# Optimization experiments

Measured on AMD Instinct MI355X. Metric: run time of the kernel, lower is better.

The kernel has to match this reference:

```python
import jax, jax.numpy as jnp
import numpy as np

N = 20000      # atoms
E = 320000     # edges
F = 128        # node_size (hard-pinned by split(128) / expand to 384)
RBF = 20
RC = 5.0
ITERS = 3
NM = 64        # molecules in batch


def setup_inputs() -> dict:
    key = jax.random.key(0)
    ks = iter(jax.random.split(key, 64))
    def nrm(shape, scale=0.05):
        return jax.random.normal(next(ks), shape, dtype=jnp.float32) * scale
    inp = {}
    inp["z"] = jax.random.randint(next(ks), (N,), 0, 119)
    inp["graph"] = jax.random.randint(next(ks), (E, 2), 0, N)
    inp["edges_dist"] = jax.random.uniform(next(ks), (E,), minval=0.5, maxval=RC, dtype=jnp.float32)
    sense = jax.random.normal(next(ks), (E, 3), dtype=jnp.float32)
    inp["edges_sense"] = sense / jnp.linalg.norm(sense, axis=1, keepdims=True)
    inp["graph_idx"] = jnp.sort(jax.random.randint(next(ks), (N,), 0, NM))
    # parameters (stacked over ITERS message/update blocks)
    inp["emb"] = nrm((119, F), 1.0)
    inp["mw1"] = nrm((ITERS, F, F)); inp["mb1"] = nrm((ITERS, F))
    inp["mw2"] = nrm((ITERS, 3 * F, F)); inp["mb2"] = nrm((ITERS, 3 * F))
    inp["ew"] = nrm((ITERS, 3 * F, RBF)); inp["eb"] = nrm((ITERS, 3 * F))
    inp["uw"] = nrm((ITERS, F, F)); inp["vw"] = nrm((ITERS, F, F))
    inp["aw1"] = nrm((ITERS, F, 2 * F)); inp["ab1"] = nrm((ITERS, F))
    inp["aw2"] = nrm((ITERS, 3 * F, F)); inp["ab2"] = nrm((ITERS, 3 * F))
    inp["ow1"] = nrm((F, F)); inp["ob1"] = nrm((F,))
    inp["ow2"] = nrm((1, F)); inp["ob2"] = nrm((1,))
    return inp


def reference(z, graph, edges_dist, edges_sense, graph_idx,
              emb, mw1, mb1, mw2, mb2, ew, eb,
              uw, vw, aw1, ab1, aw2, ab2, ow1, ob1, ow2, ob2):
    src = graph[:, 0]   # scatter target (index_add index)
    dst = graph[:, 1]   # gather source (neighbour)
    s = emb[z]                                  # [N, F]
    v = jnp.zeros((N, 3, F), dtype=s.dtype)     # [N, 3, F]
    # edge-level precompute (same every iteration)
    n = jnp.arange(1, RBF + 1, dtype=jnp.float32)
    d = edges_dist[:, None]
    rbf = jnp.sin(n * jnp.pi * d / RC) / d                              # [E, RBF]
    cut = 0.5 * (jnp.cos(jnp.pi * edges_dist / RC) + 1.0) * (edges_dist < RC)  # [E]
    for i in range(ITERS):
        # --- Message block ---
        a = jax.nn.silu(s @ mw1[i].T + mb1[i]) @ mw2[i].T + mb2[i]      # [N, 3F]
        dist_rep = (rbf @ ew[i].T + eb[i]) * cut[:, None]               # [E, 3F]
        res = a[dst] * dist_rep                                         # [E, 3F]
        rv, rs, rd = res[:, :F], res[:, F:2 * F], res[:, 2 * F:]
        resv = v[dst] * rv[:, None, :] + edges_sense[:, :, None] * rd[:, None, :]  # [E,3,F]
        s = s + 2.0 * jax.ops.segment_sum(rs, src, num_segments=N)
        v = v + 2.0 * jax.ops.segment_sum(resv, src, num_segments=N)
        # --- Update block ---
        Uv = v @ uw[i].T                                                # [N,3,F]
        Vv = v @ vw[i].T
        h = jnp.concatenate([s, jnp.linalg.norm(Vv, axis=1)], axis=-1)  # [N, 2F]
        a2 = jax.nn.silu(h @ aw1[i].T + ab1[i]) @ aw2[i].T + ab2[i]     # [N, 3F]
        avv, asv, ass = a2[:, :F], a2[:, F:2 * F], a2[:, 2 * F:]
        s = s + ass + asv * jnp.sum(Uv * Vv, axis=1)
        v = v + avv[:, None, :] * Uv
    out = jax.nn.silu(s @ ow1.T + ob1) @ ow2.T + ob2                    # [N, 1]
    return jax.ops.segment_sum(out, graph_idx, num_segments=NM)         # [NM, 1]
```

## Files before the change

### kernel.cpp

```cpp
#include <hip/hip_runtime.h>
#include <math.h>

#define NN 20000
#define NE 320000
#define FD 128
#define RBFN 20
#define RC_ 5.0f
#define NITER 3
#define NMOL 64
#define F3 384
#define F2 256
#define PI_ 3.14159265358979323846f
#define KB 128
#define LPAD 8
#define SDS 392

typedef __attribute__((ext_vector_type(8))) short  bf16x8;
typedef __attribute__((ext_vector_type(4))) float  floatx4;
typedef unsigned short u16;
typedef unsigned int   u32;

__device__ __forceinline__ u16 f2b(float x) {
    union { float f; unsigned int u; } v; v.f = x;
    unsigned int u = v.u;
    return (u16)((u + 0x7fffu + ((u >> 16) & 1u)) >> 16);
}
__device__ __forceinline__ float b2f(u16 x) {
    union { unsigned int u; float f; } v; v.u = ((unsigned int)x) << 16;
    return v.f;
}
__device__ __forceinline__ float blo(u32 w) {
    union { unsigned int u; float f; } v; v.u = w << 16; return v.f;
}
__device__ __forceinline__ float bhi(u32 w) {
    union { unsigned int u; float f; } v; v.u = w & 0xffff0000u; return v.f;
}
__device__ __forceinline__ u32 pack2(float a, float b) {
    return (u32)f2b(a) | ((u32)f2b(b) << 16);
}

__global__ __launch_bounds__(256) void cvt_w_kernel(
    const float* s0, int n0, const float* s1, int n1, const float* s2, int n2,
    const float* s3, int n3, const float* s4, int n4, const float* s5, int n5,
    const float* s6, int n6, u16* __restrict__ dst)
{
    int idx = blockIdx.x * 256 + threadIdx.x;
    if (idx < n0) { dst[idx] = f2b(s0[idx]); return; } idx -= n0; dst += n0;
    if (idx < n1) { dst[idx] = f2b(s1[idx]); return; } idx -= n1; dst += n1;
    if (idx < n2) { dst[idx] = f2b(s2[idx]); return; } idx -= n2; dst += n2;
    if (idx < n3) { dst[idx] = f2b(s3[idx]); return; } idx -= n3; dst += n3;
    if (idx < n4) { dst[idx] = f2b(s4[idx]); return; } idx -= n4; dst += n4;
    if (idx < n5) { dst[idx] = f2b(s5[idx]); return; } idx -= n5; dst += n5;
    if (idx < n6) { dst[idx] = f2b(s6[idx]); }
}

__global__ __launch_bounds__(256) void cvt_ew_kernel(const float* __restrict__ ew,
    u16* __restrict__ ewb)
{
    int idx = blockIdx.x * 256 + threadIdx.x;
    if (idx >= NITER * F3 * 32) return;
    int k = idx & 31;
    int row = idx >> 5;
    ewb[idx] = (k < RBFN) ? f2b(ew[row * RBFN + k]) : (u16)0;
}

__global__ __launch_bounds__(256) void init_kernel(const int* __restrict__ z,
    const float* __restrict__ emb, float* __restrict__ s, u16* __restrict__ sbf,
    float* __restrict__ v_a, int* __restrict__ v_pk_i)
{
    int idx = blockIdx.x * 256 + threadIdx.x;
    if (idx < NN * F3) v_a[idx] = 0.f;
    if (idx < NN * F3 / 2) v_pk_i[idx] = 0;
    if (idx < NN * FD) {
        int n = idx >> 7, f = idx & 127;
        float v = emb[z[n] * FD + f];
        s[idx] = v; sbf[idx] = f2b(v);
    }
}

__global__ __launch_bounds__(256) void zero_i_kernel(int* __restrict__ p, int n)
{
    int idx = blockIdx.x * 256 + threadIdx.x;
    if (idx < n) p[idx] = 0;
}

__global__ __launch_bounds__(256) void csr_count_kernel(const int* __restrict__ graph,
    int* __restrict__ cnt)
{
    int e = blockIdx.x * 256 + threadIdx.x;
    if (e >= NE) return;
    atomicAdd(&cnt[graph[2 * e]], 1);
}

__global__ __launch_bounds__(1024) void csr_scan_kernel(const int* __restrict__ cnt,
    int* __restrict__ row_ptr, int* __restrict__ cursor)
{
    __shared__ int sd[1024];
    int tid = threadIdx.x;
    const int chunk = (NN + 1023) / 1024;
    int start = tid * chunk;
    int end = start + chunk; if (end > NN) end = NN;
    int sum = 0;
    for (int j = start; j < end; j++) sum += cnt[j];
    sd[tid] = sum;
    __syncthreads();
    for (int off = 1; off < 1024; off <<= 1) {
        int v = 0;
        if (tid >= off) v = sd[tid - off];
        __syncthreads();
        if (tid >= off) sd[tid] += v;
        __syncthreads();
    }
    int run = (tid == 0) ? 0 : sd[tid - 1];
    for (int j = start; j < end; j++) {
        row_ptr[j] = run;
        cursor[j]  = run;
        run += cnt[j];
    }
    if (tid == 0) row_ptr[NN] = NE;
}

__global__ __launch_bounds__(256) void csr_scatter_kernel(const int* __restrict__ graph,
    int* __restrict__ cursor, int* __restrict__ edge_list)
{
    int e = blockIdx.x * 256 + threadIdx.x;
    if (e >= NE) return;
    int p = atomicAdd(&cursor[graph[2 * e]], 1);
    edge_list[p] = e;
}

__global__ __launch_bounds__(256) void edge_stream_kernel(
    const int* __restrict__ edge_list, const int* __restrict__ graph,
    const float* __restrict__ dist, const float* __restrict__ sense,
    u16* __restrict__ rbf_bf, float* __restrict__ cut_p,
    float* __restrict__ sense_p, int* __restrict__ dst_p)
{
    int j = blockIdx.x * 256 + threadIdx.x;
    if (j >= NE) return;
    int e = edge_list[j];
    float d = dist[e];
    float inv = 1.f / d;
    float base = PI_ * d / RC_;
    float s1, c1;
    __sincosf(base, &s1, &c1);
    float twoc = c1 + c1;
    u16* rb = rbf_bf + (size_t)j * 32;
    float sprev = 0.f, scur = s1;
    #pragma unroll
    for (int k = 0; k < RBFN; k++) {
        rb[k] = f2b(scur * inv);
        float snext = twoc * scur - sprev;
        sprev = scur; scur = snext;
    }
    #pragma unroll
    for (int k = RBFN; k < 32; k++) rb[k] = 0;
    cut_p[j] = 0.5f * (c1 + 1.f) * (d < RC_ ? 1.f : 0.f);
    dst_p[j] = graph[2 * e + 1];
    sense_p[3 * j + 0] = sense[3 * e + 0];
    sense_p[3 * j + 1] = sense[3 * e + 1];
    sense_p[3 * j + 2] = sense[3 * e + 2];
}

template<int K1, bool PACK>
__global__ __launch_bounds__(256) void mlp_kernel(const u16* __restrict__ A,
    const u16* __restrict__ W1, const float* __restrict__ b1,
    const u16* __restrict__ W2, const float* __restrict__ b2,
    u16* __restrict__ Ob, int M)
{
    __shared__ u16 As[64][KB + LPAD];
    __shared__ u16 Ws[128][KB + LPAD];
    __shared__ u16 T[64][KB + LPAD];
    const int bm = blockIdx.x * 64;
    const int tid = threadIdx.x;
    const int wave = tid >> 6, lane = tid & 63;
    const int wm  = (wave >> 1) * 32;
    const int wn1 = (wave & 1) * 64;
    const int wn  = (wave & 1) * 32;
    const int quad = lane >> 4, lr = lane & 15;
    const int r = tid >> 2, q = tid & 3;

    floatx4 acc1[2][4];
    #pragma unroll
    for (int i = 0; i < 2; i++)
        #pragma unroll
        for (int j = 0; j < 4; j++) acc1[i][j] = (floatx4)0.f;

    for (int ko = 0; ko < K1; ko += KB) {
        {
            int gm = bm + r;
            u16* dA = &As[r][q * 32];
            if (gm < M) {
                const u16* ap = A + (size_t)gm * K1 + ko + q * 32;
                #pragma unroll
                for (int x = 0; x < 32; x += 8)
                    *(bf16x8*)&dA[x] = *(const bf16x8*)(ap + x);
            } else {
                #pragma unroll
                for (int x = 0; x < 32; x += 8)
                    *(bf16x8*)&dA[x] = (bf16x8)0;
            }
            #pragma unroll
            for (int h = 0; h < 2; h++) {
                int wr = r + h * 64;
                const u16* wp = W1 + (size_t)wr * K1 + ko + q * 32;
                u16* dW = &Ws[wr][q * 32];
                #pragma unroll
                for (int x = 0; x < 32; x += 8)
                    *(bf16x8*)&dW[x] = *(const bf16x8*)(wp + x);
            }
        }
        __syncthreads();
        #pragma unroll
        for (int kk = 0; kk < KB; kk += 32) {
            bf16x8 a0 = *(const bf16x8*)&As[wm + lr     ][kk + quad * 8];
            bf16x8 a1 = *(const bf16x8*)&As[wm + 16 + lr][kk + quad * 8];
            #pragma unroll
            for (int j = 0; j < 4; j++) {
                bf16x8 b = *(const bf16x8*)&Ws[wn1 + j * 16 + lr][kk + quad * 8];
                acc1[0][j] = __builtin_amdgcn_mfma_f32_16x16x32_bf16(a0, b, acc1[0][j], 0, 0, 0);
                acc1[1][j] = __builtin_amdgcn_mfma_f32_16x16x32_bf16(a1, b, acc1[1][j], 0, 0, 0);
            }
        }
        __syncthreads();
    }
    #pragma unroll
    for (int i = 0; i < 2; i++) {
        #pragma unroll
        for (int j = 0; j < 4; j++) {
            int col = wn1 + j * 16 + lr;
            float bb = b1[col];
            #pragma unroll
            for (int rr = 0; rr < 4; rr++) {
                int row = wm + i * 16 + quad * 4 + rr;
                float v = acc1[i][j][rr] + bb;
                v = v / (1.f + __expf(-v));
                T[row][col] = f2b(v);
            }
        }
    }
    __syncthreads();

    for (int c0 = 0; c0 < F3; c0 += 64) {
        {
            const u16* wp = W2 + (size_t)(c0 + r) * KB + q * 32;
            u16* dW = &Ws[r][q * 32];
            #pragma unroll
            for (int x = 0; x < 32; x += 8)
                *(bf16x8*)&dW[x] = *(const bf16x8*)(wp + x);
        }
        __syncthreads();
        floatx4 acc2[2][2];
        #pragma unroll
        for (int i = 0; i < 2; i++)
            #pragma unroll
            for (int j = 0; j < 2; j++) acc2[i][j] = (floatx4)0.f;
        #pragma unroll
        for (int kk = 0; kk < KB; kk += 32) {
            bf16x8 a0 = *(const bf16x8*)&T[wm + lr     ][kk + quad * 8];
            bf16x8 a1 = *(const bf16x8*)&T[wm + 16 + lr][kk + quad * 8];
            bf16x8 b0 = *(const bf16x8*)&Ws[wn + lr     ][kk + quad * 8];
            bf16x8 b1 = *(const bf16x8*)&Ws[wn + 16 + lr][kk + quad * 8];
            acc2[0][0] = __builtin_amdgcn_mfma_f32_16x16x32_bf16(a0, b0, acc2[0][0], 0, 0, 0);
            acc2[0][1] = __builtin_amdgcn_mfma_f32_16x16x32_bf16(a0, b1, acc2[0][1], 0, 0, 0);
            acc2[1][0] = __builtin_amdgcn_mfma_f32_16x16x32_bf16(a1, b0, acc2[1][0], 0, 0, 0);
            acc2[1][1] = __builtin_amdgcn_mfma_f32_16x16x32_bf16(a1, b1, acc2[1][1], 0, 0, 0);
        }
        #pragma unroll
        for (int i = 0; i < 2; i++) {
            #pragma unroll
            for (int j = 0; j < 2; j++) {
                int gn = c0 + wn + j * 16 + lr;
                float bb = b2[gn];
                #pragma unroll
                for (int rr = 0; rr < 4; rr++) {
                    int gm = bm + wm + i * 16 + quad * 4 + rr;
                    if (gm < M) {
                        u16 val = f2b(acc2[i][j][rr] + bb);
                        if (PACK) {
                            int off = (gn < 256) ? ((gn & 127) * 2 + (gn >> 7))
                                                 : (256 + (gn & 127));
                            Ob[(size_t)gm * F3 + off] = val;
                        } else {
                            Ob[(size_t)gm * F3 + gn] = val;
                        }
                    }
                }
            }
        }
        __syncthreads();
    }
}

__global__ __launch_bounds__(256) void gemm_uv(const u16* __restrict__ A,
    const u16* __restrict__ Wu, const u16* __restrict__ Wv,
    u16* __restrict__ U, u16* __restrict__ V, int M)
{
    __shared__ u16 As[64][KB + LPAD];
    __shared__ u16 Bu[64][KB + LPAD];
    __shared__ u16 Bv[64][KB + LPAD];
    const int bm = blockIdx.x * 64;
    const int bn = blockIdx.y * 64;
    const int tid = threadIdx.x;
    const int r = tid >> 2;
    const int q = tid & 3;
    const int wave = tid >> 6;
    const int lane = tid & 63;
    const int wm = (wave >> 1) * 32;
    const int wn = (wave & 1) * 32;
    const int quad = lane >> 4;
    const int lr = lane & 15;

    floatx4 au[2][2], av[2][2];
    #pragma unroll
    for (int i = 0; i < 2; i++)
        #pragma unroll
        for (int j = 0; j < 2; j++) { au[i][j] = (floatx4)0.f; av[i][j] = (floatx4)0.f; }

    {
        int gm = bm + r;
        u16* dA = &As[r][q * 32];
        if (gm < M) {
            const u16* ap = A + (size_t)gm * KB + q * 32;
            #pragma unroll
            for (int x = 0; x < 32; x += 8)
                *(bf16x8*)&dA[x] = *(const bf16x8*)(ap + x);
        } else {
            #pragma unroll
            for (int x = 0; x < 32; x += 8)
                *(bf16x8*)&dA[x] = (bf16x8)0;
        }
        int gn = bn + r;
        const u16* up = Wu + (size_t)gn * KB + q * 32;
        const u16* vp = Wv + (size_t)gn * KB + q * 32;
        u16* dU = &Bu[r][q * 32];
        u16* dV = &Bv[r][q * 32];
        #pragma unroll
        for (int x = 0; x < 32; x += 8) {
            *(bf16x8*)&dU[x] = *(const bf16x8*)(up + x);
            *(bf16x8*)&dV[x] = *(const bf16x8*)(vp + x);
        }
    }
    __syncthreads();
    #pragma unroll
    for (int kk = 0; kk < KB; kk += 32) {
        bf16x8 a0 = *(const bf16x8*)&As[wm + lr     ][kk + quad * 8];
        bf16x8 a1 = *(const bf16x8*)&As[wm + 16 + lr][kk + quad * 8];
        bf16x8 u0 = *(const bf16x8*)&Bu[wn + lr     ][kk + quad * 8];
        bf16x8 u1 = *(const bf16x8*)&Bu[wn + 16 + lr][kk + quad * 8];
        bf16x8 v0 = *(const bf16x8*)&Bv[wn + lr     ][kk + quad * 8];
        bf16x8 v1 = *(const bf16x8*)&Bv[wn + 16 + lr][kk + quad * 8];
        au[0][0] = __builtin_amdgcn_mfma_f32_16x16x32_bf16(a0, u0, au[0][0], 0, 0, 0);
        au[0][1] = __builtin_amdgcn_mfma_f32_16x16x32_bf16(a0, u1, au[0][1], 0, 0, 0);
        au[1][0] = __builtin_amdgcn_mfma_f32_16x16x32_bf16(a1, u0, au[1][0], 0, 0, 0);
        au[1][1] = __builtin_amdgcn_mfma_f32_16x16x32_bf16(a1, u1, au[1][1], 0, 0, 0);
        av[0][0] = __builtin_amdgcn_mfma_f32_16x16x32_bf16(a0, v0, av[0][0], 0, 0, 0);
        av[0][1] = __builtin_amdgcn_mfma_f32_16x16x32_bf16(a0, v1, av[0][1], 0, 0, 0);
        av[1][0] = __builtin_amdgcn_mfma_f32_16x16x32_bf16(a1, v0, av[1][0], 0, 0, 0);
        av[1][1] = __builtin_amdgcn_mfma_f32_16x16x32_bf16(a1, v1, av[1][1], 0, 0, 0);
    }
    #pragma unroll
    for (int i = 0; i < 2; i++) {
        #pragma unroll
        for (int j = 0; j < 2; j++) {
            int gn = bn + wn + j * 16 + lr;
            #pragma unroll
            for (int rr = 0; rr < 4; rr++) {
                int gm = bm + wm + i * 16 + quad * 4 + rr;
                if (gm < M) {
                    U[(size_t)gm * FD + gn] = f2b(au[i][j][rr]);
                    V[(size_t)gm * FD + gn] = f2b(av[i][j][rr]);
                }
            }
        }
    }
}

__global__ __launch_bounds__(256) void edge_mfma_kernel(
    const u16* __restrict__ rbf_bf, const float* __restrict__ cut_p,
    const float* __restrict__ sense_p, const int* __restrict__ dst_p,
    const u16* __restrict__ ewb, const float* __restrict__ eb,
    const u16* __restrict__ a_pk, const float* __restrict__ s_in,
    const float* __restrict__ v_in, const u16* __restrict__ v_pk,
    const int* __restrict__ row_ptr,
    float* __restrict__ s_out, u16* __restrict__ s_obf,
    float* __restrict__ v_out, u16* __restrict__ v_obf)
{
    __shared__ u16   sdrep[16 * SDS];
    __shared__ float scut[16];
    __shared__ float ssen[16][4];
    __shared__ int   sdst[16];
    __shared__ float red[4 * 128];

    const int n = blockIdx.x;
    const int tid = threadIdx.x;
    const int wave = tid >> 6;
    const int lane = tid & 63;
    const int quad = lane >> 4;
    const int lr = lane & 15;
    const int f = tid & 127;
    const int half = tid >> 7;

    int beg = row_ptr[n], end = row_ptr[n + 1];
    float accs = 0.f, accv0 = 0.f, accv1 = 0.f, accv2 = 0.f;

    for (int t0 = beg; t0 < end; t0 += 16) {
        int cnt = end - t0; if (cnt > 16) cnt = 16;
        __syncthreads();
        if (tid < 16) {
            scut[tid] = (tid < cnt) ? cut_p[t0 + tid] : 0.f;
            sdst[tid] = (tid < cnt) ? dst_p[t0 + tid] : 0;
        }
        if (tid >= 64 && tid < 64 + 3 * cnt) {
            int x = tid - 64;
            ssen[x / 3][x % 3] = sense_p[3 * t0 + x];
        }
        bf16x8 afrag;
        int ge = t0 + lr;
        if (ge < end) afrag = *(const bf16x8*)&rbf_bf[(size_t)ge * 32 + quad * 8];
        else          afrag = (bf16x8)0;
        floatx4 dacc[6];
        #pragma unroll
        for (int nt = 0; nt < 6; nt++) {
            int nrow = (wave * 6 + nt) * 16 + lr;
            bf16x8 bfrag = *(const bf16x8*)&ewb[(size_t)nrow * 32 + quad * 8];
            dacc[nt] = __builtin_amdgcn_mfma_f32_16x16x32_bf16(afrag, bfrag, (floatx4)0.f, 0, 0, 0);
        }
        __syncthreads();
        #pragma unroll
        for (int nt = 0; nt < 6; nt++) {
            int ncol = (wave * 6 + nt) * 16 + lr;
            float ebn = eb[ncol];
            #pragma unroll
            for (int rr = 0; rr < 4; rr++) {
                int e = quad * 4 + rr;
                sdrep[e * SDS + ncol] = f2b((dacc[nt][rr] + ebn) * scut[e]);
            }
        }
        __syncthreads();
        int nh = cnt - half * 8; if (nh > 8) nh = 8;
        for (int k = 0; k < nh; k++) {
            int e = half * 8 + k;
            int dst = sdst[e];
            const u16* sr = &sdrep[e * SDS];
            float drv = b2f(sr[f]);
            float drs = b2f(sr[FD + f]);
            float drd = b2f(sr[2 * FD + f]);
            const u16* ar = a_pk + (size_t)dst * F3;
            u32 ap = *(const u32*)(ar + f * 2);
            float rv = b2f((u16)(ap & 0xffff)) * drv;
            float rs = b2f((u16)(ap >> 16))    * drs;
            float rd = b2f(ar[256 + f])        * drd;
            accs += rs;
            const u16* vr = v_pk + (size_t)dst * F3;
            u32 vp = *(const u32*)(vr + f * 2);
            accv0 += b2f((u16)(vp & 0xffff)) * rv + ssen[e][0] * rd;
            accv1 += b2f((u16)(vp >> 16))    * rv + ssen[e][1] * rd;
            accv2 += b2f(vr[256 + f])        * rv + ssen[e][2] * rd;
        }
    }
    __syncthreads();
    if (half == 1) {
        red[f] = accs; red[128 + f] = accv0; red[256 + f] = accv1; red[384 + f] = accv2;
    }
    __syncthreads();
    if (half == 0) {
        accs  += red[f];       accv0 += red[128 + f];
        accv1 += red[256 + f]; accv2 += red[384 + f];
        int nb = n * FD + f;
        float so = s_in[nb] + 2.f * accs;
        s_out[nb] = so; s_obf[nb] = f2b(so);
        int vb = n * F3 + f;
        float w0 = v_in[vb]           + 2.f * accv0;
        float w1 = v_in[vb + FD]      + 2.f * accv1;
        float w2 = v_in[vb + 2 * FD]  + 2.f * accv2;
        v_out[vb]          = w0; v_obf[vb]          = f2b(w0);
        v_out[vb + FD]     = w1; v_obf[vb + FD]     = f2b(w1);
        v_out[vb + 2 * FD] = w2; v_obf[vb + 2 * FD] = f2b(w2);
    }
}

__global__ __launch_bounds__(256) void mlp2_update_kernel(
    const u16* __restrict__ sbf_mid, const float* __restrict__ s_mid,
    const float* __restrict__ v_mid,
    const u16* __restrict__ Uv, const u16* __restrict__ Vv,
    const u16* __restrict__ W1, const float* __restrict__ b1,
    const u16* __restrict__ W2, const float* __restrict__ b2,
    float* __restrict__ s_out, u16* __restrict__ s_obf,
    float* __restrict__ v_out, u16* __restrict__ v_pk, int M)
{
    __shared__ u16 As[64][KB + LPAD];
    __shared__ u16 Ws[128][KB + LPAD];
    __shared__ u16 T[64][KB + LPAD];
    const int bm = blockIdx.x * 64;
    const int tid = threadIdx.x;
    const int wave = tid >> 6, lane = tid & 63;
    const int wm  = (wave >> 1) * 32;
    const int wn1 = (wave & 1) * 64;
    const int wn  = (wave & 1) * 32;
    const int quad = lane >> 4, lr = lane & 15;
    const int r = tid >> 2, q = tid & 3;

    floatx4 acc1[2][4];
    #pragma unroll
    for (int i = 0; i < 2; i++)
        #pragma unroll
        for (int j = 0; j < 4; j++) acc1[i][j] = (floatx4)0.f;

    {
        int gm = bm + r;
        u16* dA = &As[r][q * 32];
        if (gm < M) {
            const u16* ap = sbf_mid + (size_t)gm * FD + q * 32;
            #pragma unroll
            for (int x = 0; x < 32; x += 8)
                *(bf16x8*)&dA[x] = *(const bf16x8*)(ap + x);
        } else {
            #pragma unroll
            for (int x = 0; x < 32; x += 8)
                *(bf16x8*)&dA[x] = (bf16x8)0;
        }
        #pragma unroll
        for (int h = 0; h < 2; h++) {
            int wr = r + h * 64;
            const u16* wp = W1 + (size_t)wr * F2 + q * 32;
            u16* dW = &Ws[wr][q * 32];
            #pragma unroll
            for (int x = 0; x < 32; x += 8)
                *(bf16x8*)&dW[x] = *(const bf16x8*)(wp + x);
        }
    }
    __syncthreads();
    #pragma unroll
    for (int kk = 0; kk < KB; kk += 32) {
        bf16x8 a0 = *(const bf16x8*)&As[wm + lr     ][kk + quad * 8];
        bf16x8 a1 = *(const bf16x8*)&As[wm + 16 + lr][kk + quad * 8];
        #pragma unroll
        for (int j = 0; j < 4; j++) {
            bf16x8 b = *(const bf16x8*)&Ws[wn1 + j * 16 + lr][kk + quad * 8];
            acc1[0][j] = __builtin_amdgcn_mfma_f32_16x16x32_bf16(a0, b, acc1[0][j], 0, 0, 0);
            acc1[1][j] = __builtin_amdgcn_mfma_f32_16x16x32_bf16(a1, b, acc1[1][j], 0, 0, 0);
        }
    }
    __syncthreads();
    {
        int gm = bm + r;
        u16* dA = &As[r][q * 32];
        if (gm < M) {
            const u16* vvp = Vv + (size_t)gm * F3 + q * 32;
            bf16x8 c0[4], c1[4], c2[4];
            #pragma unroll
            for (int t = 0; t < 4; t++) {
                c0[t] = *(const bf16x8*)(vvp + t * 8);
                c1[t] = *(const bf16x8*)(vvp + FD + t * 8);
                c2[t] = *(const bf16x8*)(vvp + 2 * FD + t * 8);
            }
            #pragma unroll
            for (int t = 0; t < 4; t++) {
                #pragma unroll
                for (int x = 0; x < 8; x++) {
                    float a = b2f((u16)c0[t][x]);
                    float b = b2f((u16)c1[t][x]);
                    float c = b2f((u16)c2[t][x]);
                    dA[t * 8 + x] = f2b(sqrtf(a * a + b * b + c * c));
                }
            }
        } else {
            #pragma unroll
            for (int x = 0; x < 32; x += 8)
                *(bf16x8*)&dA[x] = (bf16x8)0;
        }
        #pragma unroll
        for (int h = 0; h < 2; h++) {
            int wr = r + h * 64;
            const u16* wp = W1 + (size_t)wr * F2 + KB + q * 32;
            u16* dW = &Ws[wr][q * 32];
            #pragma unroll
            for (int x = 0; x < 32; x += 8)
                *(bf16x8*)&dW[x] = *(const bf16x8*)(wp + x);
        }
    }
    __syncthreads();
    #pragma unroll
    for (int kk = 0; kk < KB; kk += 32) {
        bf16x8 a0 = *(const bf16x8*)&As[wm + lr     ][kk + quad * 8];
        bf16x8 a1 = *(const bf16x8*)&As[wm + 16 + lr][kk + quad * 8];
        #pragma unroll
        for (int j = 0; j < 4; j++) {
            bf16x8 b = *(const bf16x8*)&Ws[wn1 + j * 16 + lr][kk + quad * 8];
            acc1[0][j] = __builtin_amdgcn_mfma_f32_16x16x32_bf16(a0, b, acc1[0][j], 0, 0, 0);
            acc1[1][j] = __builtin_amdgcn_mfma_f32_16x16x32_bf16(a1, b, acc1[1][j], 0, 0, 0);
        }
    }
    __syncthreads();
    #pragma unroll
    for (int i = 0; i < 2; i++) {
        #pragma unroll
        for (int j = 0; j < 4; j++) {
            int col = wn1 + j * 16 + lr;
            float bb = b1[col];
            #pragma unroll
            for (int rr = 0; rr < 4; rr++) {
                int row = wm + i * 16 + quad * 4 + rr;
                float v = acc1[i][j][rr] + bb;
                v = v / (1.f + __expf(-v));
                T[row][col] = f2b(v);
            }
        }
    }
    __syncthreads();

    float avvr[2][2][4], asvr[2][2][4];
    #pragma unroll
    for (int part = 0; part < 2; part++) {
        #pragma unroll
        for (int piece = 0; piece < 3; piece++) {
            const int c0 = piece * 128 + part * 64;
            {
                const u16* wp = W2 + (size_t)(c0 + r) * KB + q * 32;
                u16* dW = &Ws[r][q * 32];
                #pragma unroll
                for (int x = 0; x < 32; x += 8)
                    *(bf16x8*)&dW[x] = *(const bf16x8*)(wp + x);
            }
            __syncthreads();
            floatx4 acc2[2][2];
            #pragma unroll
            for (int i = 0; i < 2; i++)
                #pragma unroll
                for (int j = 0; j < 2; j++) acc2[i][j] = (floatx4)0.f;
            #pragma unroll
            for (int kk = 0; kk < KB; kk += 32) {
                bf16x8 a0 = *(const bf16x8*)&T[wm + lr     ][kk + quad * 8];
                bf16x8 a1 = *(const bf16x8*)&T[wm + 16 + lr][kk + quad * 8];
                bf16x8 b0 = *(const bf16x8*)&Ws[wn + lr     ][kk + quad * 8];
                bf16x8 b1 = *(const bf16x8*)&Ws[wn + 16 + lr][kk + quad * 8];
                acc2[0][0] = __builtin_amdgcn_mfma_f32_16x16x32_bf16(a0, b0, acc2[0][0], 0, 0, 0);
                acc2[0][1] = __builtin_amdgcn_mfma_f32_16x16x32_bf16(a0, b1, acc2[0][1], 0, 0, 0);
                acc2[1][0] = __builtin_amdgcn_mfma_f32_16x16x32_bf16(a1, b0, acc2[1][0], 0, 0, 0);
                acc2[1][1] = __builtin_amdgcn_mfma_f32_16x16x32_bf16(a1, b1, acc2[1][1], 0, 0, 0);
            }
            if (piece == 0) {
                #pragma unroll
                for (int i = 0; i < 2; i++)
                    #pragma unroll
                    for (int j = 0; j < 2; j++) {
                        int gn = c0 + wn + j * 16 + lr;
                        float bb = b2[gn];
                        #pragma unroll
                        for (int rr = 0; rr < 4; rr++)
                            avvr[i][j][rr] = acc2[i][j][rr] + bb;
                    }
            } else if (piece == 1) {
                #pragma unroll
                for (int i = 0; i < 2; i++)
                    #pragma unroll
                    for (int j = 0; j < 2; j++) {
                        int gn = c0 + wn + j * 16 + lr;
                        float bb = b2[gn];
                        #pragma unroll
                        for (int rr = 0; rr < 4; rr++)
                            asvr[i][j][rr] = acc2[i][j][rr] + bb;
                    }
            } else {
                #pragma unroll
                for (int i = 0; i < 2; i++) {
                    #pragma unroll
                    for (int j = 0; j < 2; j++) {
                        int gn = c0 + wn + j * 16 + lr;
                        int f  = gn - 256;
                        float bb = b2[gn];
                        #pragma unroll
                        for (int rr = 0; rr < 4; rr++) {
                            int gm = bm + wm + i * 16 + quad * 4 + rr;
                            if (gm < M) {
                                float ass = acc2[i][j][rr] + bb;
                                float asv = asvr[i][j][rr];
                                float avv = avvr[i][j][rr];
                                int vb = gm * F3 + f;
                                float u0 = b2f(Uv[vb]);
                                float u1 = b2f(Uv[vb + FD]);
                                float u2 = b2f(Uv[vb + 2 * FD]);
                                float w0 = b2f(Vv[vb]);
                                float w1 = b2f(Vv[vb + FD]);
                                float w2 = b2f(Vv[vb + 2 * FD]);
                                float dot = u0 * w0 + u1 * w1 + u2 * w2;
                                int nb = gm * FD + f;
                                float so = s_mid[nb] + ass + asv * dot;
                                s_out[nb] = so; s_obf[nb] = f2b(so);
                                float y0 = v_mid[vb]          + avv * u0;
                                float y1 = v_mid[vb + FD]     + avv * u1;
                                float y2 = v_mid[vb + 2 * FD] + avv * u2;
                                v_out[vb]          = y0;
                                v_out[vb + FD]     = y1;
                                v_out[vb + 2 * FD] = y2;
                                char* vpb = (char*)v_pk + (size_t)gm * (2 * F3);
                                *(u32*)(vpb + 4 * f) = pack2(y0, y1);
                                *(u16*)(vpb + 512 + 2 * f) = f2b(y2);
                            }
                        }
                    }
                }
            }
            __syncthreads();
        }
    }
}

__global__ __launch_bounds__(256) void head_kernel(const u16* __restrict__ A,
    const u16* __restrict__ W1, const float* __restrict__ b1,
    const float* __restrict__ ow2, const float* __restrict__ ob2,
    float* __restrict__ nodeval)
{
    __shared__ u16 As[64][KB + LPAD];
    __shared__ u16 Ws[128][KB + LPAD];
    __shared__ float T[64][KB + 4];
    __shared__ float ow2s[KB];
    const int bm = blockIdx.x * 64;
    const int tid = threadIdx.x;
    const int wave = tid >> 6, lane = tid & 63;
    const int wm  = (wave >> 1) * 32;
    const int wn1 = (wave & 1) * 64;
    const int quad = lane >> 4, lr = lane & 15;
    const int r = tid >> 2, q = tid & 3;

    if (tid < KB) ow2s[tid] = ow2[tid];

    floatx4 acc1[2][4];
    #pragma unroll
    for (int i = 0; i < 2; i++)
        #pragma unroll
        for (int j = 0; j < 4; j++) acc1[i][j] = (floatx4)0.f;

    {
        int gm = bm + r;
        u16* dA = &As[r][q * 32];
        if (gm < NN) {
            const u16* ap = A + (size_t)gm * KB + q * 32;
            #pragma unroll
            for (int x = 0; x < 32; x += 8)
                *(bf16x8*)&dA[x] = *(const bf16x8*)(ap + x);
        } else {
            #pragma unroll
            for (int x = 0; x < 32; x += 8)
                *(bf16x8*)&dA[x] = (bf16x8)0;
        }
        #pragma unroll
        for (int h = 0; h < 2; h++) {
            int wr = r + h * 64;
            const u16* wp = W1 + (size_t)wr * KB + q * 32;
            u16* dW = &Ws[wr][q * 32];
            #pragma unroll
            for (int x = 0; x < 32; x += 8)
                *(bf16x8*)&dW[x] = *(const bf16x8*)(wp + x);
        }
    }
    __syncthreads();
    #pragma unroll
    for (int kk = 0; kk < KB; kk += 32) {
        bf16x8 a0 = *(const bf16x8*)&As[wm + lr     ][kk + quad * 8];
        bf16x8 a1 = *(const bf16x8*)&As[wm + 16 + lr][kk + quad * 8];
        #pragma unroll
        for (int j = 0; j < 4; j++) {
            bf16x8 b = *(const bf16x8*)&Ws[wn1 + j * 16 + lr][kk + quad * 8];
            acc1[0][j] = __builtin_amdgcn_mfma_f32_16x16x32_bf16(a0, b, acc1[0][j], 0, 0, 0);
            acc1[1][j] = __builtin_amdgcn_mfma_f32_16x16x32_bf16(a1, b, acc1[1][j], 0, 0, 0);
        }
    }
    #pragma unroll
    for (int i = 0; i < 2; i++) {
        #pragma unroll
        for (int j = 0; j < 4; j++) {
            int col = wn1 + j * 16 + lr;
            float bb = b1[col];
            #pragma unroll
            for (int rr = 0; rr < 4; rr++) {
                int row = wm + i * 16 + quad * 4 + rr;
                float v = acc1[i][j][rr] + bb;
                v = v / (1.f + __expf(-v));
                T[row][col] = v;
            }
        }
    }
    __syncthreads();
    int nl = tid >> 2, seg = tid & 3;
    float v = 0.f;
    #pragma unroll
    for (int x = 0; x < 32; x++) {
        int col = seg * 32 + x;
        v += T[nl][col] * ow2s[col];
    }
    v += __shfl_down(v, 2);
    v += __shfl_down(v, 1);
    if (seg == 0) {
        int gm = bm + nl;
        if (gm < NN) nodeval[gm] = v + ob2[0];
    }
}

__global__ __launch_bounds__(1024) void mol_reduce_kernel(const float* __restrict__ nodeval,
    const int* __restrict__ gidx, float* __restrict__ out)
{
    __shared__ float mol[NMOL];
    int tid = threadIdx.x;
    if (tid < NMOL) mol[tid] = 0.f;
    __syncthreads();
    int cur = -1; float acc = 0.f;
    for (int x = tid; x < NN; x += 1024) {
        int g = gidx[x];
        float v = nodeval[x];
        if (g != cur) {
            if (cur >= 0) atomicAdd(&mol[cur], acc);
            cur = g; acc = v;
        } else acc += v;
    }
    if (cur >= 0) atomicAdd(&mol[cur], acc);
    __syncthreads();
    if (tid < NMOL) out[tid] = mol[tid];
}

extern "C" void kernel_launch(void* const* d_in, const int* in_sizes, int n_in,
                              void* d_out, int out_size, void* d_ws, size_t ws_size,
                              hipStream_t stream)
{
    const int*   z     = (const int*)d_in[0];
    const int*   graph = (const int*)d_in[1];
    const float* dist  = (const float*)d_in[2];
    const float* sense = (const float*)d_in[3];
    const int*   gidx  = (const int*)d_in[4];
    const float* emb   = (const float*)d_in[5];
    const float* mw1   = (const float*)d_in[6];
    const float* mb1   = (const float*)d_in[7];
    const float* mw2   = (const float*)d_in[8];
    const float* mb2   = (const float*)d_in[9];
    const float* ew    = (const float*)d_in[10];
    const float* eb    = (const float*)d_in[11];
    const float* uw    = (const float*)d_in[12];
    const float* vw    = (const float*)d_in[13];
    const float* aw1   = (const float*)d_in[14];
    const float* ab1   = (const float*)d_in[15];
    const float* aw2   = (const float*)d_in[16];
    const float* ab2   = (const float*)d_in[17];
    const float* ow1   = (const float*)d_in[18];
    const float* ob1   = (const float*)d_in[19];
    const float* ow2   = (const float*)d_in[20];
    const float* ob2   = (const float*)d_in[21];
    float* out = (float*)d_out;

    float* W = (float*)d_ws;
    float* s_a    = W; W += (size_t)NN * FD;
    float* s_b    = W; W += (size_t)NN * FD;
    float* v_a    = W; W += (size_t)NN * F3;
    float* v_b    = W; W += (size_t)NN * F3;
    float* cut_p  = W; W += (size_t)NE;
    float* sns_p  = W; W += (size_t)NE * 3;
    float* nodeval= W; W += (size_t)NN;
    u16* U = (u16*)W;
    u16* sbf_a = U; U += (size_t)NN * FD;
    u16* sbf_b = U; U += (size_t)NN * FD;
    u16* vbf_b = U; U += (size_t)NN * F3;
    u16* a_pk  = U; U += (size_t)NN * F3;
    u16* v_pk  = U; U += (size_t)NN * F3;
    u16* h_bf  = U; U += (size_t)NN * F2;
    u16* a2_bf = U; U += (size_t)NN * F3;
    u16* Uv_bf = U; U += (size_t)NN * F3;
    u16* Vv_bf = U; U += (size_t)NN * F3;
    u16* rbf_bf= U; U += (size_t)NE * 32;
    u16* ewb   = U; U += (size_t)NITER * F3 * 32;
    u16* wb    = U; U += 557056;
    int* ip = (int*)U;
    int* row_ptr   = ip; ip += NN + 1;
    int* cnt       = ip; ip += NN;
    int* cursor    = ip; ip += NN;
    int* edge_list = ip; ip += NE;
    int* dst_p     = ip; ip += NE;

    u16* wb_mw1 = wb;
    u16* wb_mw2 = wb + 49152;
    u16* wb_uw  = wb + 196608;
    u16* wb_vw  = wb + 245760;
    u16* wb_aw1 = wb + 294912;
    u16* wb_aw2 = wb + 393216;
    u16* wb_ow1 = wb + 540672;
    const int WTOT = 557056;

    const int TB = 256;
    dim3 b256(TB);

    cvt_w_kernel<<<dim3((WTOT + TB - 1) / TB), b256, 0, stream>>>(
        mw1, 49152, mw2, 147456, uw, 49152, vw, 49152, aw1, 98304, aw2, 147456,
        ow1, 16384, wb);
    cvt_ew_kernel<<<dim3((NITER * F3 * 32 + TB - 1) / TB), b256, 0, stream>>>(ew, ewb);
    init_kernel<<<dim3((NN * F3 + TB - 1) / TB), b256, 0, stream>>>(
        z, emb, s_a, sbf_a, v_a, (int*)v_pk);
    zero_i_kernel<<<dim3((NN + TB - 1) / TB), b256, 0, stream>>>(cnt, NN);
    csr_count_kernel<<<dim3((NE + TB - 1) / TB), b256, 0, stream>>>(graph, cnt);
    csr_scan_kernel<<<dim3(1), dim3(1024), 0, stream>>>(cnt, row_ptr, cursor);
    csr_scatter_kernel<<<dim3((NE + TB - 1) / TB), b256, 0, stream>>>(graph, cursor, edge_list);
    edge_stream_kernel<<<dim3((NE + TB - 1) / TB), b256, 0, stream>>>(
        edge_list, graph, dist, sense, rbf_bf, cut_p, sns_p, dst_p);

    dim3 gM((NN + 63) / 64);
    dim3 gV2((3 * NN + 63) / 64, FD / 64);

    for (int i = 0; i < NITER; i++) {
        mlp_kernel<128, true><<<gM, b256, 0, stream>>>(sbf_a,
            wb_mw1 + (size_t)i * FD * FD, mb1 + (size_t)i * FD,
            wb_mw2 + (size_t)i * F3 * FD, mb2 + (size_t)i * F3, a_pk, NN);
        edge_mfma_kernel<<<dim3(NN), b256, 0, stream>>>(
            rbf_bf, cut_p, sns_p, dst_p,
            ewb + (size_t)i * F3 * 32, eb + (size_t)i * F3,
            a_pk, s_a, v_a, v_pk, row_ptr, s_b, sbf_b, v_b, vbf_b);
        gemm_uv<<<gV2, b256, 0, stream>>>(vbf_b, wb_uw + (size_t)i * FD * FD,
            wb_vw + (size_t)i * FD * FD, Uv_bf, Vv_bf, 3 * NN);
        mlp2_update_kernel<<<gM, b256, 0, stream>>>(
            sbf_b, s_b, v_b, Uv_bf, Vv_bf,
            wb_aw1 + (size_t)i * FD * F2, ab1 + (size_t)i * FD,
            wb_aw2 + (size_t)i * F3 * FD, ab2 + (size_t)i * F3,
            s_a, sbf_a, v_a, v_pk, NN);
    }

    head_kernel<<<gM, b256, 0, stream>>>(sbf_a, wb_ow1, ob1, ow2, ob2, nodeval);
    mol_reduce_kernel<<<dim3(1), dim3(1024), 0, stream>>>(nodeval, gidx, out);
}
```

Baseline: 873.0 us.

## Fuse next-iteration message MLP and output head into update kernel; merge init kernels

The update kernel now keeps the new bf16 scalar features in shared memory and runs the next iteration's message MLP (or, on the last iteration, the output head MLP) directly on them. This removes the separate mlp_kernel launches for later iterations, the head kernel, and the global round-trip of sbf. The four setup kernels (weight conversion, ew conversion, state init, count zeroing) are merged into one launch. In exchange the fused kernel uses more registers and shared memory, and its extra work runs serially inside each block.

```diff
diff --git a/kernel.cpp b/kernel.cpp
--- a/kernel.cpp
+++ b/kernel.cpp
@@ -39,49 +39,40 @@
     return (u32)f2b(a) | ((u32)f2b(b) << 16);
 }
 
-__global__ __launch_bounds__(256) void cvt_w_kernel(
+__global__ __launch_bounds__(256) void init_all_kernel(
     const float* s0, int n0, const float* s1, int n1, const float* s2, int n2,
     const float* s3, int n3, const float* s4, int n4, const float* s5, int n5,
-    const float* s6, int n6, u16* __restrict__ dst)
-{
-    int idx = blockIdx.x * 256 + threadIdx.x;
-    if (idx < n0) { dst[idx] = f2b(s0[idx]); return; } idx -= n0; dst += n0;
-    if (idx < n1) { dst[idx] = f2b(s1[idx]); return; } idx -= n1; dst += n1;
-    if (idx < n2) { dst[idx] = f2b(s2[idx]); return; } idx -= n2; dst += n2;
-    if (idx < n3) { dst[idx] = f2b(s3[idx]); return; } idx -= n3; dst += n3;
-    if (idx < n4) { dst[idx] = f2b(s4[idx]); return; } idx -= n4; dst += n4;
-    if (idx < n5) { dst[idx] = f2b(s5[idx]); return; } idx -= n5; dst += n5;
-    if (idx < n6) { dst[idx] = f2b(s6[idx]); }
-}
-
-__global__ __launch_bounds__(256) void cvt_ew_kernel(const float* __restrict__ ew,
-    u16* __restrict__ ewb)
-{
-    int idx = blockIdx.x * 256 + threadIdx.x;
-    if (idx >= NITER * F3 * 32) return;
-    int k = idx & 31;
-    int row = idx >> 5;
-    ewb[idx] = (k < RBFN) ? f2b(ew[row * RBFN + k]) : (u16)0;
-}
-
-__global__ __launch_bounds__(256) void init_kernel(const int* __restrict__ z,
-    const float* __restrict__ emb, float* __restrict__ s, u16* __restrict__ sbf,
-    float* __restrict__ v_a, int* __restrict__ v_pk_i)
+    const float* s6, int n6, u16* __restrict__ wdst,
+    const float* __restrict__ ew, u16* __restrict__ ewb,
+    const int* __restrict__ z, const float* __restrict__ emb,
+    float* __restrict__ s, u16* __restrict__ sbf,
+    float* __restrict__ v_a, int* __restrict__ v_pk_i, int* __restrict__ cnt)
 {
     int idx = blockIdx.x * 256 + threadIdx.x;
     if (idx < NN * F3) v_a[idx] = 0.f;
     if (idx < NN * F3 / 2) v_pk_i[idx] = 0;
+    if (idx < NN) cnt[idx] = 0;
     if (idx < NN * FD) {
         int n = idx >> 7, f = idx & 127;
         float v = emb[z[n] * FD + f];
         s[idx] = v; sbf[idx] = f2b(v);
     }
-}
-
-__global__ __launch_bounds__(256) void zero_i_kernel(int* __restrict__ p, int n)
-{
-    int idx = blockIdx.x * 256 + threadIdx.x;
-    if (idx < n) p[idx] = 0;
+    if (idx < NITER * F3 * 32) {
+        int k = idx & 31;
+        int row = idx >> 5;
+        ewb[idx] = (k < RBFN) ? f2b(ew[row * RBFN + k]) : (u16)0;
+    }
+    {
+        int w = idx;
+        u16* dst = wdst;
+        if (w < n0) { dst[w] = f2b(s0[w]); return; } w -= n0; dst += n0;
+        if (w < n1) { dst[w] = f2b(s1[w]); return; } w -= n1; dst += n1;
+        if (w < n2) { dst[w] = f2b(s2[w]); return; } w -= n2; dst += n2;
+        if (w < n3) { dst[w] = f2b(s3[w]); return; } w -= n3; dst += n3;
+        if (w < n4) { dst[w] = f2b(s4[w]); return; } w -= n4; dst += n4;
+        if (w < n5) { dst[w] = f2b(s5[w]); return; } w -= n5; dst += n5;
+        if (w < n6) { dst[w] = f2b(s6[w]); }
+    }
 }
 
 __global__ __launch_bounds__(256) void csr_count_kernel(const int* __restrict__ graph,
@@ -479,14 +470,21 @@
     }
 }
 
-__global__ __launch_bounds__(256) void mlp2_update_kernel(
+template<bool LAST>
+__global__ __launch_bounds__(256) void mlp2_update_next_kernel(
     const u16* __restrict__ sbf_mid, const float* __restrict__ s_mid,
     const float* __restrict__ v_mid,
     const u16* __restrict__ Uv, const u16* __restrict__ Vv,
     const u16* __restrict__ W1, const float* __restrict__ b1,
     const u16* __restrict__ W2, const float* __restrict__ b2,
-    float* __restrict__ s_out, u16* __restrict__ s_obf,
-    float* __restrict__ v_out, u16* __restrict__ v_pk, int M)
+    float* __restrict__ s_out,
+    float* __restrict__ v_out, u16* __restrict__ v_pk,
+    const u16* __restrict__ N_W1, const float* __restrict__ N_b1,
+    const u16* __restrict__ N_W2, const float* __restrict__ N_b2,
+    u16* __restrict__ a_pk,
+    const u16* __restrict__ H_W1, const float* __restrict__ H_b1,
+    const float* __restrict__ ow2, const float* __restrict__ ob2,
+    float* __restrict__ nodeval, int M)
 {
     __shared__ u16 As[64][KB + LPAD];
     __shared__ u16 Ws[128][KB + LPAD];
@@ -671,7 +669,8 @@
                         float bb = b2[gn];
                         #pragma unroll
                         for (int rr = 0; rr < 4; rr++) {
-                            int gm = bm + wm + i * 16 + quad * 4 + rr;
+                            int row = wm + i * 16 + quad * 4 + rr;
+                            int gm = bm + row;
                             if (gm < M) {
                                 float ass = acc2[i][j][rr] + bb;
                                 float asv = asvr[i][j][rr];
@@ -686,7 +685,8 @@
                                 float dot = u0 * w0 + u1 * w1 + u2 * w2;
                                 int nb = gm * FD + f;
                                 float so = s_mid[nb] + ass + asv * dot;
-                                s_out[nb] = so; s_obf[nb] = f2b(so);
+                                s_out[nb] = so;
+                                As[row][f] = f2b(so);
                                 float y0 = v_mid[vb]          + avv * u0;
                                 float y1 = v_mid[vb + FD]     + avv * u1;
                                 float y2 = v_mid[vb + 2 * FD] + avv * u2;
@@ -696,6 +696,8 @@
                                 char* vpb = (char*)v_pk + (size_t)gm * (2 * F3);
                                 *(u32*)(vpb + 4 * f) = pack2(y0, y1);
                                 *(u16*)(vpb + 512 + 2 * f) = f2b(y2);
+                            } else {
+                                As[row][f] = 0;
                             }
                         }
                     }
@@ -704,96 +706,158 @@
             __syncthreads();
         }
     }
-}
-
-__global__ __launch_bounds__(256) void head_kernel(const u16* __restrict__ A,
-    const u16* __restrict__ W1, const float* __restrict__ b1,
-    const float* __restrict__ ow2, const float* __restrict__ ob2,
-    float* __restrict__ nodeval)
-{
-    __shared__ u16 As[64][KB + LPAD];
-    __shared__ u16 Ws[128][KB + LPAD];
-    __shared__ float T[64][KB + 4];
-    __shared__ float ow2s[KB];
-    const int bm = blockIdx.x * 64;
-    const int tid = threadIdx.x;
-    const int wave = tid >> 6, lane = tid & 63;
-    const int wm  = (wave >> 1) * 32;
-    const int wn1 = (wave & 1) * 64;
-    const int quad = lane >> 4, lr = lane & 15;
-    const int r = tid >> 2, q = tid & 3;
-
-    if (tid < KB) ow2s[tid] = ow2[tid];
-
-    floatx4 acc1[2][4];
-    #pragma unroll
-    for (int i = 0; i < 2; i++)
-        #pragma unroll
-        for (int j = 0; j < 4; j++) acc1[i][j] = (floatx4)0.f;
-
-    {
-        int gm = bm + r;
-        u16* dA = &As[r][q * 32];
-        if (gm < NN) {
-            const u16* ap = A + (size_t)gm * KB + q * 32;
-            #pragma unroll
-            for (int x = 0; x < 32; x += 8)
-                *(bf16x8*)&dA[x] = *(const bf16x8*)(ap + x);
-        } else {
-            #pragma unroll
-            for (int x = 0; x < 32; x += 8)
-                *(bf16x8*)&dA[x] = (bf16x8)0;
-        }
-        #pragma unroll
-        for (int h = 0; h < 2; h++) {
-            int wr = r + h * 64;
-            const u16* wp = W1 + (size_t)wr * KB + q * 32;
-            u16* dW = &Ws[wr][q * 32];
-            #pragma unroll
-            for (int x = 0; x < 32; x += 8)
-                *(bf16x8*)&dW[x] = *(const bf16x8*)(wp + x);
-        }
-    }
-    __syncthreads();
-    #pragma unroll
-    for (int kk = 0; kk < KB; kk += 32) {
-        bf16x8 a0 = *(const bf16x8*)&As[wm + lr     ][kk + quad * 8];
-        bf16x8 a1 = *(const bf16x8*)&As[wm + 16 + lr][kk + quad * 8];
-        #pragma unroll
-        for (int j = 0; j < 4; j++) {
-            bf16x8 b = *(const bf16x8*)&Ws[wn1 + j * 16 + lr][kk + quad * 8];
-            acc1[0][j] = __builtin_amdgcn_mfma_f32_16x16x32_bf16(a0, b, acc1[0][j], 0, 0, 0);
-            acc1[1][j] = __builtin_amdgcn_mfma_f32_16x16x32_bf16(a1, b, acc1[1][j], 0, 0, 0);
-        }
-    }
-    #pragma unroll
-    for (int i = 0; i < 2; i++) {
-        #pragma unroll
-        for (int j = 0; j < 4; j++) {
-            int col = wn1 + j * 16 + lr;
-            float bb = b1[col];
-            #pragma unroll
-            for (int rr = 0; rr < 4; rr++) {
-                int row = wm + i * 16 + quad * 4 + rr;
-                float v = acc1[i][j][rr] + bb;
-                v = v / (1.f + __expf(-v));
-                T[row][col] = v;
-            }
-        }
-    }
-    __syncthreads();
-    int nl = tid >> 2, seg = tid & 3;
-    float v = 0.f;
-    #pragma unroll
-    for (int x = 0; x < 32; x++) {
-        int col = seg * 32 + x;
-        v += T[nl][col] * ow2s[col];
-    }
-    v += __shfl_down(v, 2);
-    v += __shfl_down(v, 1);
-    if (seg == 0) {
-        int gm = bm + nl;
-        if (gm < NN) nodeval[gm] = v + ob2[0];
+
+    if constexpr (!LAST) {
+        {
+            #pragma unroll
+            for (int h = 0; h < 2; h++) {
+                int wr = r + h * 64;
+                const u16* wp = N_W1 + (size_t)wr * KB + q * 32;
+                u16* dW = &Ws[wr][q * 32];
+                #pragma unroll
+                for (int x = 0; x < 32; x += 8)
+                    *(bf16x8*)&dW[x] = *(const bf16x8*)(wp + x);
+            }
+        }
+        __syncthreads();
+        #pragma unroll
+        for (int i = 0; i < 2; i++)
+            #pragma unroll
+            for (int j = 0; j < 4; j++) acc1[i][j] = (floatx4)0.f;
+        #pragma unroll
+        for (int kk = 0; kk < KB; kk += 32) {
+            bf16x8 a0 = *(const bf16x8*)&As[wm + lr     ][kk + quad * 8];
+            bf16x8 a1 = *(const bf16x8*)&As[wm + 16 + lr][kk + quad * 8];
+            #pragma unroll
+            for (int j = 0; j < 4; j++) {
+                bf16x8 b = *(const bf16x8*)&Ws[wn1 + j * 16 + lr][kk + quad * 8];
+                acc1[0][j] = __builtin_amdgcn_mfma_f32_16x16x32_bf16(a0, b, acc1[0][j], 0, 0, 0);
+                acc1[1][j] = __builtin_amdgcn_mfma_f32_16x16x32_bf16(a1, b, acc1[1][j], 0, 0, 0);
+            }
+        }
+        __syncthreads();
+        #pragma unroll
+        for (int i = 0; i < 2; i++) {
+            #pragma unroll
+            for (int j = 0; j < 4; j++) {
+                int col = wn1 + j * 16 + lr;
+                float bb = N_b1[col];
+                #pragma unroll
+                for (int rr = 0; rr < 4; rr++) {
+                    int row = wm + i * 16 + quad * 4 + rr;
+                    float v = acc1[i][j][rr] + bb;
+                    v = v / (1.f + __expf(-v));
+                    T[row][col] = f2b(v);
+                }
+            }
+        }
+        __syncthreads();
+        for (int c0 = 0; c0 < F3; c0 += 64) {
+            {
+                const u16* wp = N_W2 + (size_t)(c0 + r) * KB + q * 32;
+                u16* dW = &Ws[r][q * 32];
+                #pragma unroll
+                for (int x = 0; x < 32; x += 8)
+                    *(bf16x8*)&dW[x] = *(const bf16x8*)(wp + x);
+            }
+            __syncthreads();
+            floatx4 acc2[2][2];
+            #pragma unroll
+            for (int i = 0; i < 2; i++)
+                #pragma unroll
+                for (int j = 0; j < 2; j++) acc2[i][j] = (floatx4)0.f;
+            #pragma unroll
+            for (int kk = 0; kk < KB; kk += 32) {
+                bf16x8 a0 = *(const bf16x8*)&T[wm + lr     ][kk + quad * 8];
+                bf16x8 a1 = *(const bf16x8*)&T[wm + 16 + lr][kk + quad * 8];
+                bf16x8 b0 = *(const bf16x8*)&Ws[wn + lr     ][kk + quad * 8];
+                bf16x8 b1 = *(const bf16x8*)&Ws[wn + 16 + lr][kk + quad * 8];
+                acc2[0][0] = __builtin_amdgcn_mfma_f32_16x16x32_bf16(a0, b0, acc2[0][0], 0, 0, 0);
+                acc2[0][1] = __builtin_amdgcn_mfma_f32_16x16x32_bf16(a0, b1, acc2[0][1], 0, 0, 0);
+                acc2[1][0] = __builtin_amdgcn_mfma_f32_16x16x32_bf16(a1, b0, acc2[1][0], 0, 0, 0);
+                acc2[1][1] = __builtin_amdgcn_mfma_f32_16x16x32_bf16(a1, b1, acc2[1][1], 0, 0, 0);
+            }
+            #pragma unroll
+            for (int i = 0; i < 2; i++) {
+                #pragma unroll
+                for (int j = 0; j < 2; j++) {
+                    int gn = c0 + wn + j * 16 + lr;
+                    float bb = N_b2[gn];
+                    #pragma unroll
+                    for (int rr = 0; rr < 4; rr++) {
+                        int gm = bm + wm + i * 16 + quad * 4 + rr;
+                        if (gm < M) {
+                            u16 val = f2b(acc2[i][j][rr] + bb);
+                            int off = (gn < 256) ? ((gn & 127) * 2 + (gn >> 7))
+                                                 : (256 + (gn & 127));
+                            a_pk[(size_t)gm * F3 + off] = val;
+                        }
+                    }
+                }
+            }
+            __syncthreads();
+        }
+    } else {
+        {
+            #pragma unroll
+            for (int h = 0; h < 2; h++) {
+                int wr = r + h * 64;
+                const u16* wp = H_W1 + (size_t)wr * KB + q * 32;
+                u16* dW = &Ws[wr][q * 32];
+                #pragma unroll
+                for (int x = 0; x < 32; x += 8)
+                    *(bf16x8*)&dW[x] = *(const bf16x8*)(wp + x);
+            }
+        }
+        __syncthreads();
+        #pragma unroll
+        for (int i = 0; i < 2; i++)
+            #pragma unroll
+            for (int j = 0; j < 4; j++) acc1[i][j] = (floatx4)0.f;
+        #pragma unroll
+        for (int kk = 0; kk < KB; kk += 32) {
+            bf16x8 a0 = *(const bf16x8*)&As[wm + lr     ][kk + quad * 8];
+            bf16x8 a1 = *(const bf16x8*)&As[wm + 16 + lr][kk + quad * 8];
+            #pragma unroll
+            for (int j = 0; j < 4; j++) {
+                bf16x8 b = *(const bf16x8*)&Ws[wn1 + j * 16 + lr][kk + quad * 8];
+                acc1[0][j] = __builtin_amdgcn_mfma_f32_16x16x32_bf16(a0, b, acc1[0][j], 0, 0, 0);
+                acc1[1][j] = __builtin_amdgcn_mfma_f32_16x16x32_bf16(a1, b, acc1[1][j], 0, 0, 0);
+            }
+        }
+        __syncthreads();
+        float* Tf   = (float*)&Ws[0][0];
+        float* ow2s = (float*)&As[0][0];
+        if (tid < KB) ow2s[tid] = ow2[tid];
+        #pragma unroll
+        for (int i = 0; i < 2; i++) {
+            #pragma unroll
+            for (int j = 0; j < 4; j++) {
+                int col = wn1 + j * 16 + lr;
+                float bb = H_b1[col];
+                #pragma unroll
+                for (int rr = 0; rr < 4; rr++) {
+                    int row = wm + i * 16 + quad * 4 + rr;
+                    float v = acc1[i][j][rr] + bb;
+                    v = v / (1.f + __expf(-v));
+                    Tf[row * 132 + col] = v;
+                }
+            }
+        }
+        __syncthreads();
+        int nl = tid >> 2, seg = tid & 3;
+        float v = 0.f;
+        #pragma unroll
+        for (int x = 0; x < 32; x++) {
+            int col = seg * 32 + x;
+            v += Tf[nl * 132 + col] * ow2s[col];
+        }
+        v += __shfl_down(v, 2);
+        v += __shfl_down(v, 1);
+        if (seg == 0) {
+            int gm = bm + nl;
+            if (gm < M) nodeval[gm] = v + ob2[0];
+        }
     }
 }
 
@@ -881,18 +945,13 @@
     u16* wb_aw1 = wb + 294912;
     u16* wb_aw2 = wb + 393216;
     u16* wb_ow1 = wb + 540672;
-    const int WTOT = 557056;
 
     const int TB = 256;
     dim3 b256(TB);
 
-    cvt_w_kernel<<<dim3((WTOT + TB - 1) / TB), b256, 0, stream>>>(
+    init_all_kernel<<<dim3((NN * F3 + TB - 1) / TB), b256, 0, stream>>>(
         mw1, 49152, mw2, 147456, uw, 49152, vw, 49152, aw1, 98304, aw2, 147456,
-        ow1, 16384, wb);
-    cvt_ew_kernel<<<dim3((NITER * F3 * 32 + TB - 1) / TB), b256, 0, stream>>>(ew, ewb);
-    init_kernel<<<dim3((NN * F3 + TB - 1) / TB), b256, 0, stream>>>(
-        z, emb, s_a, sbf_a, v_a, (int*)v_pk);
-    zero_i_kernel<<<dim3((NN + TB - 1) / TB), b256, 0, stream>>>(cnt, NN);
+        ow1, 16384, wb, ew, ewb, z, emb, s_a, sbf_a, v_a, (int*)v_pk, cnt);
     csr_count_kernel<<<dim3((NE + TB - 1) / TB), b256, 0, stream>>>(graph, cnt);
     csr_scan_kernel<<<dim3(1), dim3(1024), 0, stream>>>(cnt, row_ptr, cursor);
     csr_scatter_kernel<<<dim3((NE + TB - 1) / TB), b256, 0, stream>>>(graph, cursor, edge_list);
@@ -902,23 +961,35 @@
     dim3 gM((NN + 63) / 64);
     dim3 gV2((3 * NN + 63) / 64, FD / 64);
 
+    mlp_kernel<128, true><<<gM, b256, 0, stream>>>(sbf_a,
+        wb_mw1, mb1, wb_mw2, mb2, a_pk, NN);
+
     for (int i = 0; i < NITER; i++) {
-        mlp_kernel<128, true><<<gM, b256, 0, stream>>>(sbf_a,
-            wb_mw1 + (size_t)i * FD * FD, mb1 + (size_t)i * FD,
-            wb_mw2 + (size_t)i * F3 * FD, mb2 + (size_t)i * F3, a_pk, NN);
         edge_mfma_kernel<<<dim3(NN), b256, 0, stream>>>(
             rbf_bf, cut_p, sns_p, dst_p,
             ewb + (size_t)i * F3 * 32, eb + (size_t)i * F3,
             a_pk, s_a, v_a, v_pk, row_ptr, s_b, sbf_b, v_b, vbf_b);
         gemm_uv<<<gV2, b256, 0, stream>>>(vbf_b, wb_uw + (size_t)i * FD * FD,
             wb_vw + (size_t)i * FD * FD, Uv_bf, Vv_bf, 3 * NN);
-        mlp2_update_kernel<<<gM, b256, 0, stream>>>(
-            sbf_b, s_b, v_b, Uv_bf, Vv_bf,
-            wb_aw1 + (size_t)i * FD * F2, ab1 + (size_t)i * FD,
-            wb_aw2 + (size_t)i * F3 * FD, ab2 + (size_t)i * F3,
-            s_a, sbf_a, v_a, v_pk, NN);
-    }
-
-    head_kernel<<<gM, b256, 0, stream>>>(sbf_a, wb_ow1, ob1, ow2, ob2, nodeval);
+        if (i < NITER - 1) {
+            mlp2_update_next_kernel<false><<<gM, b256, 0, stream>>>(
+                sbf_b, s_b, v_b, Uv_bf, Vv_bf,
+                wb_aw1 + (size_t)i * FD * F2, ab1 + (size_t)i * FD,
+                wb_aw2 + (size_t)i * F3 * FD, ab2 + (size_t)i * F3,
+                s_a, v_a, v_pk,
+                wb_mw1 + (size_t)(i + 1) * FD * FD, mb1 + (size_t)(i + 1) * FD,
+                wb_mw2 + (size_t)(i + 1) * F3 * FD, mb2 + (size_t)(i + 1) * F3, a_pk,
+                nullptr, nullptr, nullptr, nullptr, nullptr, NN);
+        } else {
+            mlp2_update_next_kernel<true><<<gM, b256, 0, stream>>>(
+                sbf_b, s_b, v_b, Uv_bf, Vv_bf,
+                wb_aw1 + (size_t)i * FD * F2, ab1 + (size_t)i * FD,
+                wb_aw2 + (size_t)i * F3 * FD, ab2 + (size_t)i * F3,
+                s_a, v_a, v_pk,
+                nullptr, nullptr, nullptr, nullptr, nullptr,
+                wb_ow1, ob1, ow2, ob2, nodeval, NN);
+        }
+    }
+
     mol_reduce_kernel<<<dim3(1), dim3(1024), 0, stream>>>(nodeval, gidx, out);
 }
```

Measured after the change: 868.5 us. About the same (-0.5%).
